# Kernel optimization log

Measured on AMD Instinct MI355X. Metric: run time of the kernel, lower is better.

Reference implementation:

```python
import jax, jax.numpy as jnp
import numpy as np

NB = 5  # frequency bands


def _ln(x, g, b, eps=1e-5):
    m = jnp.mean(x, axis=-1, keepdims=True)
    v = jnp.var(x, axis=-1, keepdims=True)
    return (x - m) / jnp.sqrt(v + eps) * g + b


def _graph_adj(x, adj_w, sw1, sb1, sw2, sb2, pos_factor, pos_enc):
    # x: [B, D, N] -> degree-normalized adjacency [B, N, N]
    d = x.shape[1]
    xt = jnp.swapaxes(x, 1, 2)  # [B, N, D]
    # concat-MLP first layer split: cat(xi, xj) @ W1 == xi @ W1[:d] + xj @ W1[d:]
    a = xt @ sw1[:d]
    bpart = xt @ sw1[d:]
    h = jax.nn.elu(a[:, :, None, :] + bpart[:, None, :, :] + sb1)  # [B, N, N, H]
    dyn = jax.nn.sigmoid(jnp.squeeze(h @ sw2, -1) + sb2)  # [B, N, N]
    static = jax.nn.softmax(adj_w, axis=-1)
    pos = jax.nn.softmax(pos_enc, axis=-1)
    comb = jax.nn.softmax(static + dyn + pos_factor * pos, axis=-1)
    deg = jnp.sum(comb, axis=-1)
    dis = (deg + 1e-8) ** -0.5
    return dis[:, :, None] * comb * dis[:, None, :]


def _gcn(x, adj, w, b):
    # x: [B, D, N], adj: [B, N, N] -> [B, D_out, N]
    xt = jnp.swapaxes(x, 1, 2)
    out = jnp.einsum('bij,bjd->bid', adj, xt) @ w + b
    return jnp.swapaxes(out, 1, 2)


def _mha(x, qkv_w, qkv_b, ow, ob, nh=4):
    B, S, D = x.shape
    dh = D // nh
    q, k, v = jnp.split(x @ qkv_w + qkv_b, 3, axis=-1)
    q = q.reshape(B, S, nh, dh)
    k = k.reshape(B, S, nh, dh)
    v = v.reshape(B, S, nh, dh)
    att = jax.nn.softmax(jnp.einsum('bihd,bjhd->bhij', q, k) / float(np.sqrt(dh)), axis=-1)
    o = jnp.einsum('bhij,bjhd->bihd', att, v).reshape(B, S, D)
    return o @ ow + ob


def setup_inputs():
    key = jax.random.key(0)
    B, D, N = 16, 256, 64
    ks = iter(jax.random.split(key, 40))

    def rn(shape, s=0.05):
        return jax.random.normal(next(ks), shape, dtype=jnp.float32) * s

    eyeN = jnp.eye(N, dtype=jnp.float32)
    return dict(
        feature=jax.random.normal(next(ks), (B, NB * D, 1, N), dtype=jnp.float32),
        l_adj_w=jnp.tile(eyeN[None], (NB, 1, 1)),
        l_sim_w1=rn((NB, 2 * D, D)), l_sim_b1=jnp.zeros((NB, D), jnp.float32),
        l_sim_w2=rn((NB, D, 1)), l_sim_b2=jnp.zeros((NB, 1), jnp.float32),
        l_pos_factor=jnp.full((NB,), 0.5, jnp.float32),
        l_pos_enc=jnp.tile(eyeN[None], (NB, 1, 1)),
        l_gcn_w=rn((NB, D, D)), l_gcn_b=jnp.zeros((NB, D), jnp.float32),
        g_adj_w=jnp.eye(NB, dtype=jnp.float32),
        g_sim_w1=rn((2 * D, D)), g_sim_b1=jnp.zeros((D,), jnp.float32),
        g_sim_w2=rn((D, 1)), g_sim_b2=jnp.zeros((1,), jnp.float32),
        g_pos_factor=jnp.float32(0.5),
        g_pos_enc=jnp.eye(NB, dtype=jnp.float32),
        g_gcn_w=rn((D, D)), g_gcn_b=jnp.zeros((D,), jnp.float32),
        qkv_w=rn((D, 3 * D)), qkv_b=jnp.zeros((3 * D,), jnp.float32),
        attn_ow=rn((D, D)), attn_ob=jnp.zeros((D,), jnp.float32),
        ln1_g=jnp.ones((D,), jnp.float32), ln1_b=jnp.zeros((D,), jnp.float32),
        ln2_g=jnp.ones((D,), jnp.float32), ln2_b=jnp.zeros((D,), jnp.float32),
        mlp_w1=rn((D, 4 * D)), mlp_b1=jnp.zeros((4 * D,), jnp.float32),
        mlp_w2=rn((4 * D, D)), mlp_b2=jnp.zeros((D,), jnp.float32),
        imp_w=rn((NB, N, 1)), imp_b=jnp.zeros((NB, 1), jnp.float32),
    )


def reference(feature, l_adj_w, l_sim_w1, l_sim_b1, l_sim_w2, l_sim_b2,
              l_pos_factor, l_pos_enc, l_gcn_w, l_gcn_b,
              g_adj_w, g_sim_w1, g_sim_b1, g_sim_w2, g_sim_b2,
              g_pos_factor, g_pos_enc, g_gcn_w, g_gcn_b,
              qkv_w, qkv_b, attn_ow, attn_ob,
              ln1_g, ln1_b, ln2_g, ln2_b,
              mlp_w1, mlp_b1, mlp_w2, mlp_b2,
              imp_w, imp_b):
    B = feature.shape[0]
    D = l_gcn_w.shape[-1]
    N = feature.shape[-1]
    # [B, 5*D, 1, N] -> [5, B, D, N] band-major
    x5 = jnp.moveaxis(feature.reshape(B, NB, D, N), 1, 0)
    # per-band local graphs + GCNs (vmapped over the 5 bands)
    local_adj = jax.vmap(_graph_adj)(x5, l_adj_w, l_sim_w1, l_sim_b1,
                                     l_sim_w2, l_sim_b2, l_pos_factor, l_pos_enc)
    local_out = jax.vmap(_gcn)(x5, local_adj, l_gcn_w, l_gcn_b)  # [5, B, D, N]
    scale_nodes = jnp.moveaxis(jnp.mean(local_out, axis=-1), 0, 1)  # [B, 5, D]
    # cross-band attention block (pre: MHA + residual + LN, then MLP + residual + LN)
    attn = _mha(scale_nodes, qkv_w, qkv_b, attn_ow, attn_ob)
    h1 = _ln(scale_nodes + attn, ln1_g, ln1_b)
    mlp = jax.nn.gelu(h1 @ mlp_w1 + mlp_b1, approximate=False) @ mlp_w2 + mlp_b2
    se = _ln(h1 + mlp, ln2_g, ln2_b)  # [B, 5, D]
    # global scale graph over the 5 band nodes
    xg = jnp.swapaxes(se, 1, 2)  # [B, D, 5]
    g_adj = _graph_adj(xg, g_adj_w, g_sim_w1, g_sim_b1, g_sim_w2, g_sim_b2,
                       g_pos_factor, g_pos_enc)
    g_out = jnp.swapaxes(_gcn(xg, g_adj, g_gcn_w, g_gcn_b), 1, 2)  # [B, 5, D]
    # modulate each local band feature by its global scale vector
    enh = local_out * jnp.moveaxis(g_out, 1, 0)[..., None]  # [5, B, D, N]
    # per-band importance projection over channels: [5, B, D, 1]
    out5 = jnp.einsum('kbdn,kno->kbdo', enh, imp_w) + imp_b[:, None, None, :]
    output = jnp.moveaxis(out5, 0, 1).reshape(B, NB * D, 1, 1)
    return output, g_adj, jnp.moveaxis(local_out, 0, 1)
```

## Files before the change

### kernel.cpp

```cpp
#include <hip/hip_runtime.h>
#include <hip/hip_bf16.h>

#define NBANDS 5
#define BATCH  16
#define DIM    256
#define NNODE  64
#define SEQ    5
#define NHEAD  4
#define DHEAD  64

typedef __hip_bfloat16 bf16;
typedef unsigned short ushort_t;
typedef __attribute__((ext_vector_type(8))) short short8;
typedef __attribute__((ext_vector_type(4))) float float4v;

__device__ __forceinline__ float bu2f(ushort_t u){
    bf16 h = *reinterpret_cast<bf16*>(&u);
    return __bfloat162float(h);
}
__device__ __forceinline__ ushort_t f2bu(float x){
    bf16 h = __float2bfloat16(x);
    return *reinterpret_cast<ushort_t*>(&h);
}

__global__ void k_bases(const float* __restrict__ l_adj_w, const float* __restrict__ l_pos_enc,
                        const float* __restrict__ l_pf,
                        const float* __restrict__ g_adj_w, const float* __restrict__ g_pos_enc,
                        const float* __restrict__ g_pf,
                        float* __restrict__ sbase, float* __restrict__ gbase,
                        float* __restrict__ zbuf)
{
    int blk = blockIdx.x;
    int t = threadIdx.x;
    if (blk < NBANDS*NNODE) {
        int k = blk / NNODE, i = blk % NNODE;
        float aw = l_adj_w[(k*NNODE + i)*NNODE + t];
        float pe = l_pos_enc[(k*NNODE + i)*NNODE + t];
        float m1 = aw, m2 = pe;
        for (int o=32;o>0;o>>=1){ m1 = fmaxf(m1, __shfl_xor(m1,o,64)); m2 = fmaxf(m2, __shfl_xor(m2,o,64)); }
        float e1 = __expf(aw-m1), e2 = __expf(pe-m2);
        float s1=e1, s2=e2;
        for (int o=32;o>0;o>>=1){ s1 += __shfl_xor(s1,o,64); s2 += __shfl_xor(s2,o,64); }
        float pf = l_pf[k];
        sbase[(k*NNODE+i)*NNODE + t] = e1/s1 + pf*(e2/s2);
    } else if (blk == NBANDS*NNODE) {
        if (t < NBANDS) {
            int i = t;
            float r1[NBANDS], r2[NBANDS];
            float m1=-1e30f, m2=-1e30f;
            for (int j=0;j<NBANDS;j++){
                r1[j]=g_adj_w[i*NBANDS+j]; r2[j]=g_pos_enc[i*NBANDS+j];
                m1=fmaxf(m1,r1[j]); m2=fmaxf(m2,r2[j]);
            }
            float s1=0.f,s2=0.f;
            for (int j=0;j<NBANDS;j++){ r1[j]=__expf(r1[j]-m1); r2[j]=__expf(r2[j]-m2); s1+=r1[j]; s2+=r2[j]; }
            float pf = g_pf[0];
            for (int j=0;j<NBANDS;j++) gbase[i*NBANDS+j] = r1[j]/s1 + pf*(r2[j]/s2);
        }
    } else {
        for (int i=t;i<DIM;i+=64) zbuf[i] = 0.f;
    }
}

__global__ void k_prep(const float* __restrict__ w1, const float* __restrict__ gw,
                       ushort_t* __restrict__ w1bt, ushort_t* __restrict__ gwbt)
{
    int blk = blockIdx.x;
    int inst = blk >> 4;
    int t = blk & 15;
    int r0 = (t>>2)*64, c0 = (t&3)*64;
    const float* src; ushort_t* dst;
    if (inst < 10){
        int k = inst>>1, half = inst&1;
        src = w1  + ((size_t)k*512 + half*256)*256;
        dst = w1bt+ ((size_t)k*512 + half*256)*256;
    } else {
        int k = inst-10;
        src = gw  + (size_t)k*65536;
        dst = gwbt+ (size_t)k*65536;
    }
    __shared__ ushort_t tile[64][65];
    int tid = threadIdx.x;
    int jj = tid & 63, i4 = tid >> 6;
    for (int p=0;p<16;p++){
        int i = p*4 + i4;
        tile[i][jj] = f2bu(src[(size_t)(r0+i)*256 + c0 + jj]);
    }
    __syncthreads();
    for (int p=0;p<16;p++){
        int i = p*4 + i4;
        dst[(size_t)(c0+i)*256 + r0 + jj] = tile[jj][i];
    }
}

__global__ void k_transpose_feat(const float* __restrict__ feat,
                                 ushort_t* __restrict__ xtb,
                                 ushort_t* __restrict__ xtT)
{
    int k = blockIdx.x / BATCH, b = blockIdx.x % BATCH;
    __shared__ ushort_t tile[64][65];
    const float* src = feat + ((size_t)b*NBANDS*DIM + (size_t)k*DIM)*NNODE;
    ushort_t* dst = xtb + (size_t)(k*BATCH+b)*NNODE*DIM;
    int tid = threadIdx.x;
    ushort_t* dstT = xtT + (size_t)(k*BATCH+b)*DIM*NNODE;
    for (int u=0; u<64; ++u){
        int idx = u*256 + tid;
        dstT[idx] = f2bu(src[idx]);
    }
    for (int dt=0; dt<4; ++dt){
        for (int r=0;r<16;r++){
            int dp = r*4 + (tid>>6);
            int n  = tid & 63;
            tile[dp][n] = f2bu(src[(size_t)(dt*64+dp)*NNODE + n]);
        }
        __syncthreads();
        for (int r=0;r<16;r++){
            int n  = r*4 + (tid>>6);
            int dp = tid & 63;
            dst[(size_t)n*DIM + dt*64 + dp] = tile[dp][n];
        }
        __syncthreads();
    }
}

__global__ void __launch_bounds__(256) k_ab_mfma(const ushort_t* __restrict__ xtb,
                        const ushort_t* __restrict__ w1bt, const float* __restrict__ b1,
                        ushort_t* __restrict__ aab, ushort_t* __restrict__ bbb)
{
    int blk = blockIdx.x;
    int kband = blk / (BATCH*8);
    int b = (blk/8) % BATCH;
    int nblk = blk & 7;
    int tid = threadIdx.x;
    int wave = tid>>6, lane = tid&63;
    int c16 = lane & 15, quad = lane >> 4;
    int m0 = wave*16;
    size_t rowbase = (size_t)(kband*BATCH+b)*NNODE;
    const ushort_t* Aptr = xtb + (rowbase + m0 + c16)*DIM + quad*8;
    const ushort_t* Bbase = w1bt + (size_t)kband*512*DIM;
    int ncol0 = nblk*64;
    const ushort_t* Bptr0 = Bbase + (size_t)(ncol0 +  0 + c16)*DIM + quad*8;
    const ushort_t* Bptr1 = Bbase + (size_t)(ncol0 + 16 + c16)*DIM + quad*8;
    const ushort_t* Bptr2 = Bbase + (size_t)(ncol0 + 32 + c16)*DIM + quad*8;
    const ushort_t* Bptr3 = Bbase + (size_t)(ncol0 + 48 + c16)*DIM + quad*8;
    float4v acc0 = {0.f,0.f,0.f,0.f}, acc1 = acc0, acc2 = acc0, acc3 = acc0;
    #pragma unroll
    for (int ks=0; ks<8; ++ks){
        short8 a  = *reinterpret_cast<const short8*>(Aptr  + ks*32);
        short8 b0 = *reinterpret_cast<const short8*>(Bptr0 + ks*32);
        short8 b1v= *reinterpret_cast<const short8*>(Bptr1 + ks*32);
        short8 b2 = *reinterpret_cast<const short8*>(Bptr2 + ks*32);
        short8 b3 = *reinterpret_cast<const short8*>(Bptr3 + ks*32);
        acc0 = __builtin_amdgcn_mfma_f32_16x16x32_bf16(a, b0, acc0, 0,0,0);
        acc1 = __builtin_amdgcn_mfma_f32_16x16x32_bf16(a, b1v, acc1, 0,0,0);
        acc2 = __builtin_amdgcn_mfma_f32_16x16x32_bf16(a, b2, acc2, 0,0,0);
        acc3 = __builtin_amdgcn_mfma_f32_16x16x32_bf16(a, b3, acc3, 0,0,0);
    }
    int half = nblk >> 2;
    int cbase = (nblk & 3)*64;
    ushort_t* dst = half ? bbb : aab;
    float4v accs[4] = {acc0, acc1, acc2, acc3};
    #pragma unroll
    for (int nt=0; nt<4; ++nt){
        int cg = cbase + nt*16 + c16;
        float bias = half ? 0.f : b1[kband*DIM + cg];
        #pragma unroll
        for (int r=0;r<4;r++){
            int m = m0 + quad*4 + r;
            dst[(rowbase + m)*DIM + cg] = f2bu(accs[nt][r] + bias);
        }
    }
}

__global__ void k_dyn_comb(const ushort_t* __restrict__ aab,
                           const ushort_t* __restrict__ bbb,
                           const float* __restrict__ w2, const float* __restrict__ b2arr,
                           const float* __restrict__ sbase,
                           ushort_t* __restrict__ combb)
{
    int blk = blockIdx.x;
    int k = blk / (BATCH*16);
    int b = (blk / 16) % BATCH;
    int i0 = (blk % 16) * 4;
    int kb = k*BATCH + b;
    __shared__ float arows[4][DIM];
    __shared__ float w2s[DIM];
    __shared__ float dyn_s[4][NNODE];
    int tid = threadIdx.x;
    int wave = tid >> 6, lane = tid & 63;
    for (int r=0;r<4;r++) arows[r][tid] = bu2f(aab[((size_t)kb*NNODE + i0 + r)*DIM + tid]);
    w2s[tid] = w2[k*DIM + tid];
    __syncthreads();
    const ushort_t* bpbase = bbb + (size_t)kb*NNODE*DIM;
    for (int jt=0; jt<16; ++jt){
        int j = jt*4 + wave;
        const ushort_t* bj = bpbase + (size_t)j*DIM;
        float acc[4] = {0.f,0.f,0.f,0.f};
        #pragma unroll
        for (int m=0;m<4;m++){
            int dd = lane + m*64;
            float bpv = bu2f(bj[dd]);
            float wv  = w2s[dd];
            #pragma unroll
            for (int r=0;r<4;r++){
                float v = arows[r][dd] + bpv;
                float e = (v > 0.f) ? v : (__expf(v) - 1.f);
                acc[r] += e*wv;
            }
        }
        #pragma unroll
        for (int r=0;r<4;r++){
            float s = acc[r];
            for (int o=32;o>0;o>>=1) s += __shfl_xor(s,o,64);
            if (lane==0) dyn_s[r][j] = s;
        }
    }
    __syncthreads();
    {
        float sb2 = b2arr[k];
        float t = dyn_s[wave][lane] + sb2;
        float sg = 1.f/(1.f + __expf(-t));
        float val = sbase[(k*NNODE + i0 + wave)*NNODE + lane] + sg;
        float m = val;
        for (int o=32;o>0;o>>=1) m = fmaxf(m, __shfl_xor(m,o,64));
        float e = __expf(val - m);
        float s = e;
        for (int o=32;o>0;o>>=1) s += __shfl_xor(s,o,64);
        combb[((size_t)kb*NNODE + i0 + wave)*NNODE + lane] = f2bu(e/s);
    }
}

__global__ void __launch_bounds__(256) k_y_mfma(const ushort_t* __restrict__ combb,
                       const ushort_t* __restrict__ xtT,
                       ushort_t* __restrict__ yb)
{
    int blk = blockIdx.x;
    int kband = blk / (BATCH*4);
    int b = (blk/4) % BATCH;
    int nblk = blk & 3;
    int tid = threadIdx.x;
    int wave = tid>>6, lane = tid&63;
    int c16 = lane & 15, quad = lane >> 4;
    int m0 = wave*16;
    int kb = kband*BATCH + b;
    const ushort_t* Aptr = combb + ((size_t)kb*NNODE + m0 + c16)*NNODE + quad*8;
    const ushort_t* Bbase = xtT + (size_t)kb*DIM*NNODE;
    int ncol0 = nblk*64;
    const ushort_t* Bptr0 = Bbase + (size_t)(ncol0 +  0 + c16)*NNODE + quad*8;
    const ushort_t* Bptr1 = Bbase + (size_t)(ncol0 + 16 + c16)*NNODE + quad*8;
    const ushort_t* Bptr2 = Bbase + (size_t)(ncol0 + 32 + c16)*NNODE + quad*8;
    const ushort_t* Bptr3 = Bbase + (size_t)(ncol0 + 48 + c16)*NNODE + quad*8;
    float4v acc0 = {0.f,0.f,0.f,0.f}, acc1 = acc0, acc2 = acc0, acc3 = acc0;
    #pragma unroll
    for (int ks=0; ks<2; ++ks){
        short8 a  = *reinterpret_cast<const short8*>(Aptr  + ks*32);
        short8 b0 = *reinterpret_cast<const short8*>(Bptr0 + ks*32);
        short8 b1v= *reinterpret_cast<const short8*>(Bptr1 + ks*32);
        short8 b2 = *reinterpret_cast<const short8*>(Bptr2 + ks*32);
        short8 b3 = *reinterpret_cast<const short8*>(Bptr3 + ks*32);
        acc0 = __builtin_amdgcn_mfma_f32_16x16x32_bf16(a, b0, acc0, 0,0,0);
        acc1 = __builtin_amdgcn_mfma_f32_16x16x32_bf16(a, b1v, acc1, 0,0,0);
        acc2 = __builtin_amdgcn_mfma_f32_16x16x32_bf16(a, b2, acc2, 0,0,0);
        acc3 = __builtin_amdgcn_mfma_f32_16x16x32_bf16(a, b3, acc3, 0,0,0);
    }
    size_t rowbase = (size_t)kb*NNODE;
    float4v accs[4] = {acc0, acc1, acc2, acc3};
    #pragma unroll
    for (int nt=0; nt<4; ++nt){
        int cg = ncol0 + nt*16 + c16;
        #pragma unroll
        for (int r=0;r<4;r++){
            int m = m0 + quad*4 + r;
            yb[(rowbase + m)*DIM + cg] = f2bu(accs[nt][r]);
        }
    }
}

__global__ void __launch_bounds__(256) k_gcn_mfma(const ushort_t* __restrict__ yb,
                         const ushort_t* __restrict__ gwbt, const float* __restrict__ gb,
                         float* __restrict__ out_local)
{
    int blk = blockIdx.x;
    int kband = blk / (BATCH*4);
    int b = (blk/4) % BATCH;
    int nblk = blk & 3;
    int tid = threadIdx.x;
    int wave = tid>>6, lane = tid&63;
    int c16 = lane & 15, quad = lane >> 4;
    int m0 = wave*16;
    int kb = kband*BATCH + b;
    const ushort_t* Aptr = yb + ((size_t)kb*NNODE + m0 + c16)*DIM + quad*8;
    const ushort_t* Bbase = gwbt + (size_t)kband*DIM*DIM;
    int ncol0 = nblk*64;
    const ushort_t* Bptr0 = Bbase + (size_t)(ncol0 +  0 + c16)*DIM + quad*8;
    const ushort_t* Bptr1 = Bbase + (size_t)(ncol0 + 16 + c16)*DIM + quad*8;
    const ushort_t* Bptr2 = Bbase + (size_t)(ncol0 + 32 + c16)*DIM + quad*8;
    const ushort_t* Bptr3 = Bbase + (size_t)(ncol0 + 48 + c16)*DIM + quad*8;
    float4v acc0 = {0.f,0.f,0.f,0.f}, acc1 = acc0, acc2 = acc0, acc3 = acc0;
    #pragma unroll
    for (int ks=0; ks<8; ++ks){
        short8 a  = *reinterpret_cast<const short8*>(Aptr  + ks*32);
        short8 b0 = *reinterpret_cast<const short8*>(Bptr0 + ks*32);
        short8 b1v= *reinterpret_cast<const short8*>(Bptr1 + ks*32);
        short8 b2 = *reinterpret_cast<const short8*>(Bptr2 + ks*32);
        short8 b3 = *reinterpret_cast<const short8*>(Bptr3 + ks*32);
        acc0 = __builtin_amdgcn_mfma_f32_16x16x32_bf16(a, b0, acc0, 0,0,0);
        acc1 = __builtin_amdgcn_mfma_f32_16x16x32_bf16(a, b1v, acc1, 0,0,0);
        acc2 = __builtin_amdgcn_mfma_f32_16x16x32_bf16(a, b2, acc2, 0,0,0);
        acc3 = __builtin_amdgcn_mfma_f32_16x16x32_bf16(a, b3, acc3, 0,0,0);
    }
    float4v accs[4] = {acc0, acc1, acc2, acc3};
    #pragma unroll
    for (int nt=0; nt<4; ++nt){
        int cg = ncol0 + nt*16 + c16;
        float bias = gb[kband*DIM + cg];
        float4 v = make_float4(accs[nt][0]+bias, accs[nt][1]+bias, accs[nt][2]+bias, accs[nt][3]+bias);
        float* dst = out_local + ((size_t)(b*NBANDS + kband)*DIM + cg)*NNODE + m0 + quad*4;
        *reinterpret_cast<float4*>(dst) = v;
    }
}

__global__ void k_scale(const float* __restrict__ out_local, float* __restrict__ scalew)
{
    int k = blockIdx.x / BATCH, b = blockIdx.x % BATCH;
    int d = threadIdx.x;
    const float4* zl = reinterpret_cast<const float4*>(out_local + ((size_t)(b*NBANDS + k)*DIM + d)*NNODE);
    float acc = 0.f;
    #pragma unroll
    for (int q=0;q<16;++q){
        float4 v = zl[q];
        acc += v.x + v.y + v.z + v.w;
    }
    scalew[((size_t)b*SEQ + k)*DIM + d] = acc * (1.f/64.f);
}

template<int COLS, int SLICES>
__global__ void __launch_bounds__(256) k_gemv(const float* __restrict__ x, const float* __restrict__ w,
                       const float* __restrict__ bias, float* __restrict__ out,
                       int K, int N, int act)
{
    int chunks = N / COLS;
    int row = blockIdx.x / chunks;
    int n0 = (blockIdx.x % chunks) * COLS;
    int c = threadIdx.x % COLS, s = threadIdx.x / COLS;
    __shared__ float xs[1024];
    __shared__ float part[SLICES][COLS];
    for (int i = threadIdx.x; i < K; i += 256) xs[i] = x[(size_t)row*K + i];
    __syncthreads();
    int klen = K / SLICES;
    const float* wp = w + (size_t)(s*klen)*N + n0 + c;
    const float* xp = xs + s*klen;
    float acc = 0.f;
    #pragma unroll 8
    for (int i = 0; i < klen; ++i) acc += xp[i] * wp[(size_t)i*N];
    part[s][c] = acc;
    __syncthreads();
    if (s == 0){
        float v = bias[n0+c];
        #pragma unroll
        for (int q=0;q<SLICES;q++) v += part[q][c];
        if (act) v = 0.5f*v*(1.f + erff(v*0.70710678118654752f));
        out[(size_t)row*N + n0 + c] = v;
    }
}

__global__ void k_attn(const float* __restrict__ qkvw, float* __restrict__ ows)
{
    int b = blockIdx.x;
    int tid = threadIdx.x;
    int h = tid >> 6, l = tid & 63;
    __shared__ float att[NHEAD][SEQ][SEQ];
    const float* base = qkvw + (size_t)b*SEQ*3*DIM;
    for (int i=0;i<SEQ;i++){
        float qv = base[(size_t)i*3*DIM + h*DHEAD + l];
        for (int j=0;j<SEQ;j++){
            float kv = base[(size_t)j*3*DIM + DIM + h*DHEAD + l];
            float p = qv * kv;
            for (int o=32;o>0;o>>=1) p += __shfl_xor(p,o,64);
            if (l==0) att[h][i][j] = p * 0.125f;
        }
    }
    __syncthreads();
    if (l == 0){
        for (int i=0;i<SEQ;i++){
            float m=-1e30f;
            for (int j=0;j<SEQ;j++) m = fmaxf(m, att[h][i][j]);
            float e[SEQ]; float s=0.f;
            for (int j=0;j<SEQ;j++){ e[j] = __expf(att[h][i][j]-m); s+=e[j]; }
            for (int j=0;j<SEQ;j++) att[h][i][j] = e[j]/s;
        }
    }
    __syncthreads();
    for (int i=0;i<SEQ;i++){
        float acc=0.f;
        for (int j=0;j<SEQ;j++) acc += att[h][i][j] * base[(size_t)j*3*DIM + 2*DIM + h*DHEAD + l];
        ows[((size_t)b*SEQ + i)*DIM + h*DHEAD + l] = acc;
    }
}

__device__ __forceinline__ float block_ln(float v, int tid, float* red, float g, float bln)
{
    float s = v;
    for (int o=32;o>0;o>>=1) s += __shfl_xor(s,o,64);
    int wave = tid>>6, lane = tid&63;
    if (lane==0) red[wave] = s;
    __syncthreads();
    float mean = (red[0]+red[1]+red[2]+red[3]) * (1.f/DIM);
    float c = v - mean;
    float q = c*c;
    for (int o=32;o>0;o>>=1) q += __shfl_xor(q,o,64);
    __syncthreads();
    if (lane==0) red[wave] = q;
    __syncthreads();
    float var = (red[0]+red[1]+red[2]+red[3]) * (1.f/DIM);
    return c * rsqrtf(var + 1e-5f) * g + bln;
}

__global__ void k_ln(const float* __restrict__ a, const float* __restrict__ r,
                     const float* __restrict__ g, const float* __restrict__ be,
                     float* __restrict__ out)
{
    int row = blockIdx.x;
    int d = threadIdx.x;
    __shared__ float red[4];
    float v = a[(size_t)row*DIM + d] + r[(size_t)row*DIM + d];
    out[(size_t)row*DIM + d] = block_ln(v, d, red, g[d], be[d]);
}

__global__ void k_gadj(const float* __restrict__ gaw, const float* __restrict__ gbw,
                       const float* __restrict__ gw2, const float* __restrict__ gb2,
                       const float* __restrict__ gbase,
                       float* __restrict__ gcombw, float* __restrict__ out_gadj)
{
    int b = blockIdx.x;
    int tid = threadIdx.x;
    int wave = tid>>6, lane = tid&63;
    __shared__ float dyn[SEQ][SEQ];
    __shared__ float w2s[DIM];
    w2s[tid] = gw2[tid];
    __syncthreads();
    for (int p = wave; p < SEQ*SEQ; p += 4){
        int i = p / SEQ, j = p % SEQ;
        const float* gar = gaw + ((size_t)b*SEQ+i)*DIM;
        const float* gbr = gbw + ((size_t)b*SEQ+j)*DIM;
        float acc = 0.f;
        #pragma unroll
        for (int m=0;m<4;m++){
            int dd = lane + m*64;
            float v = gar[dd] + gbr[dd];
            float e = (v>0.f) ? v : (__expf(v)-1.f);
            acc += e * w2s[dd];
        }
        for (int o=32;o>0;o>>=1) acc += __shfl_xor(acc,o,64);
        if (lane==0) dyn[i][j] = acc;
    }
    __syncthreads();
    if (tid < SEQ){
        int i = tid;
        float sb2 = gb2[0];
        float row[SEQ]; float m=-1e30f;
        for (int j=0;j<SEQ;j++){
            float sg = 1.f/(1.f+__expf(-(dyn[i][j]+sb2)));
            row[j] = gbase[i*SEQ+j] + sg;
            m = fmaxf(m,row[j]);
        }
        float ssum=0.f;
        for (int j=0;j<SEQ;j++){ row[j]=__expf(row[j]-m); ssum+=row[j]; }
        for (int j=0;j<SEQ;j++){
            float c = row[j]/ssum;
            gcombw[((size_t)b*SEQ+i)*SEQ + j] = c;
            out_gadj[((size_t)b*SEQ+i)*SEQ + j] = c;
        }
    }
}

__global__ void k_gmix(const float* __restrict__ gcombw, const float* __restrict__ sew,
                       float* __restrict__ trow)
{
    int row = blockIdx.x;
    int b = row / SEQ;
    int d = threadIdx.x;
    float t = 0.f;
    #pragma unroll
    for (int j=0;j<SEQ;j++) t += gcombw[row*SEQ + j] * sew[((size_t)b*SEQ + j)*DIM + d];
    trow[(size_t)row*DIM + d] = t;
}

__global__ void k_final(const float* __restrict__ out_local,
                        const float* __restrict__ goutw,
                        const float* __restrict__ imp_w, const float* __restrict__ imp_b,
                        float* __restrict__ out0)
{
    int b = blockIdx.x / NBANDS, k = blockIdx.x % NBANDS;
    __shared__ float iw[NNODE];
    int d = threadIdx.x;
    if (d < NNODE) iw[d] = imp_w[k*NNODE + d];
    __syncthreads();
    const float4* zl = reinterpret_cast<const float4*>(out_local + ((size_t)(b*NBANDS + k)*DIM + d)*NNODE);
    float acc = 0.f;
    #pragma unroll
    for (int q=0;q<16;++q){
        float4 v = zl[q];
        acc += v.x*iw[q*4] + v.y*iw[q*4+1] + v.z*iw[q*4+2] + v.w*iw[q*4+3];
    }
    float val = goutw[((size_t)b*NBANDS+k)*DIM + d] * acc + imp_b[k];
    out0[((size_t)b*NBANDS+k)*DIM + d] = val;
}

extern "C" void kernel_launch(void* const* d_in, const int* in_sizes, int n_in,
                              void* d_out, int out_size, void* d_ws, size_t ws_size,
                              hipStream_t stream)
{
    const float* feature      = (const float*)d_in[0];
    const float* l_adj_w      = (const float*)d_in[1];
    const float* l_sim_w1     = (const float*)d_in[2];
    const float* l_sim_b1     = (const float*)d_in[3];
    const float* l_sim_w2     = (const float*)d_in[4];
    const float* l_sim_b2     = (const float*)d_in[5];
    const float* l_pos_factor = (const float*)d_in[6];
    const float* l_pos_enc    = (const float*)d_in[7];
    const float* l_gcn_w      = (const float*)d_in[8];
    const float* l_gcn_b      = (const float*)d_in[9];
    const float* g_adj_w      = (const float*)d_in[10];
    const float* g_sim_w1     = (const float*)d_in[11];
    const float* g_sim_b1     = (const float*)d_in[12];
    const float* g_sim_w2     = (const float*)d_in[13];
    const float* g_sim_b2     = (const float*)d_in[14];
    const float* g_pos_factor = (const float*)d_in[15];
    const float* g_pos_enc    = (const float*)d_in[16];
    const float* g_gcn_w      = (const float*)d_in[17];
    const float* g_gcn_b      = (const float*)d_in[18];
    const float* qkv_w        = (const float*)d_in[19];
    const float* qkv_b        = (const float*)d_in[20];
    const float* attn_ow      = (const float*)d_in[21];
    const float* attn_ob      = (const float*)d_in[22];
    const float* ln1_g        = (const float*)d_in[23];
    const float* ln1_b        = (const float*)d_in[24];
    const float* ln2_g        = (const float*)d_in[25];
    const float* ln2_b        = (const float*)d_in[26];
    const float* mlp_w1       = (const float*)d_in[27];
    const float* mlp_b1       = (const float*)d_in[28];
    const float* mlp_w2       = (const float*)d_in[29];
    const float* mlp_b2       = (const float*)d_in[30];
    const float* imp_w        = (const float*)d_in[31];
    const float* imp_b        = (const float*)d_in[32];

    float* out0      = (float*)d_out;
    float* out_gadj  = out0 + (size_t)BATCH*NBANDS*DIM;
    float* out_local = out_gadj + (size_t)BATCH*NBANDS*NBANDS;

    const size_t BIG = (size_t)NBANDS*BATCH*NNODE*DIM;
    ushort_t* xtb   = (ushort_t*)d_ws;
    ushort_t* aab   = xtb + BIG;
    ushort_t* bbb   = aab + BIG;
    ushort_t* xtT   = bbb + BIG;
    ushort_t* yb    = aab;
    ushort_t* w1bt  = xtT + BIG;
    ushort_t* gwbt  = w1bt + (size_t)NBANDS*512*DIM;
    ushort_t* combb = gwbt + (size_t)NBANDS*DIM*DIM;
    float* fp = (float*)(combb + (size_t)NBANDS*BATCH*NNODE*NNODE);
    float* sbase  = fp; fp += NBANDS*NNODE*NNODE;
    float* gbase  = fp; fp += 32;
    float* zbuf   = fp; fp += DIM;
    float* scalew = fp; fp += BATCH*SEQ*DIM;
    float* qkvw   = fp; fp += BATCH*SEQ*3*DIM;
    float* ows    = fp; fp += BATCH*SEQ*DIM;
    float* projw  = fp; fp += BATCH*SEQ*DIM;
    float* h1w    = fp; fp += BATCH*SEQ*DIM;
    float* mhw    = fp; fp += BATCH*SEQ*4*DIM;
    float* m2w    = fp; fp += BATCH*SEQ*DIM;
    float* sew    = fp; fp += BATCH*SEQ*DIM;
    float* gaw    = fp; fp += BATCH*SEQ*DIM;
    float* gbw    = fp; fp += BATCH*SEQ*DIM;
    float* gcombw = fp; fp += 512;
    float* trow   = fp; fp += BATCH*SEQ*DIM;
    float* goutw  = fp; fp += BATCH*SEQ*DIM;

    const int ROWS = BATCH*SEQ;

    k_bases<<<NBANDS*NNODE + 2, 64, 0, stream>>>(l_adj_w, l_pos_enc, l_pos_factor,
                                                 g_adj_w, g_pos_enc, g_pos_factor,
                                                 sbase, gbase, zbuf);
    k_prep<<<240, 256, 0, stream>>>(l_sim_w1, l_gcn_w, w1bt, gwbt);
    k_transpose_feat<<<NBANDS*BATCH, 256, 0, stream>>>(feature, xtb, xtT);
    k_ab_mfma<<<NBANDS*BATCH*8, 256, 0, stream>>>(xtb, w1bt, l_sim_b1, aab, bbb);
    k_dyn_comb<<<NBANDS*BATCH*16, 256, 0, stream>>>(aab, bbb, l_sim_w2, l_sim_b2, sbase, combb);
    k_y_mfma<<<NBANDS*BATCH*4, 256, 0, stream>>>(combb, xtT, yb);
    k_gcn_mfma<<<NBANDS*BATCH*4, 256, 0, stream>>>(yb, gwbt, l_gcn_b, out_local);
    k_scale<<<NBANDS*BATCH, 256, 0, stream>>>(out_local, scalew);
    k_gemv<64,4><<<ROWS*12, 256, 0, stream>>>(scalew, qkv_w, qkv_b, qkvw, 256, 768, 0);
    k_attn<<<BATCH, 256, 0, stream>>>(qkvw, ows);
    k_gemv<64,4><<<ROWS*4, 256, 0, stream>>>(ows, attn_ow, attn_ob, projw, 256, 256, 0);
    k_ln<<<ROWS, 256, 0, stream>>>(projw, scalew, ln1_g, ln1_b, h1w);
    k_gemv<64,4><<<ROWS*16, 256, 0, stream>>>(h1w, mlp_w1, mlp_b1, mhw, 256, 1024, 1);
    k_gemv<32,8><<<ROWS*8, 256, 0, stream>>>(mhw, mlp_w2, mlp_b2, m2w, 1024, 256, 0);
    k_ln<<<ROWS, 256, 0, stream>>>(m2w, h1w, ln2_g, ln2_b, sew);
    k_gemv<64,4><<<ROWS*4, 256, 0, stream>>>(sew, g_sim_w1, g_sim_b1, gaw, 256, 256, 0);
    k_gemv<64,4><<<ROWS*4, 256, 0, stream>>>(sew, g_sim_w1 + (size_t)DIM*DIM, zbuf, gbw, 256, 256, 0);
    k_gadj<<<BATCH, 256, 0, stream>>>(gaw, gbw, g_sim_w2, g_sim_b2, gbase, gcombw, out_gadj);
    k_gmix<<<ROWS, 256, 0, stream>>>(gcombw, sew, trow);
    k_gemv<64,4><<<ROWS*4, 256, 0, stream>>>(trow, g_gcn_w, g_gcn_b, goutw, 256, 256, 0);
    k_final<<<BATCH*NBANDS, 256, 0, stream>>>(out_local, goutw, imp_w, imp_b, out0);
}
```

Measured before the change: 264.7 us.

## Merge prep kernels into one head kernel and fuse the tail into one per-batch kernel

Three setup kernels (bases, weight transposes, feature transpose) become a single launch. That launch also converts all tail weights to bf16. The thirteen tail kernels (scale, gemvs, attention, layernorms, global adjacency, gmix, final) are fused into one kernel with one block per batch, keeping intermediates in shared memory. This removes many launches and global round trips. In exchange the tail runs on only 16 blocks, each streaming about 2MB of bf16 weights serially, and the tail weights are now rounded to bf16.

```diff
diff --git a/kernel.cpp b/kernel.cpp
--- a/kernel.cpp
+++ b/kernel.cpp
@@ -23,17 +23,29 @@
     return *reinterpret_cast<ushort_t*>(&h);
 }
 
-__global__ void k_bases(const float* __restrict__ l_adj_w, const float* __restrict__ l_pos_enc,
-                        const float* __restrict__ l_pf,
-                        const float* __restrict__ g_adj_w, const float* __restrict__ g_pos_enc,
-                        const float* __restrict__ g_pf,
-                        float* __restrict__ sbase, float* __restrict__ gbase,
-                        float* __restrict__ zbuf)
+__global__ void __launch_bounds__(256) k_head(
+    const float* __restrict__ l_adj_w, const float* __restrict__ l_pos_enc,
+    const float* __restrict__ l_pf,
+    const float* __restrict__ g_adj_w, const float* __restrict__ g_pos_enc,
+    const float* __restrict__ g_pf,
+    float* __restrict__ sbase, float* __restrict__ gbase,
+    const float* __restrict__ w1, const float* __restrict__ gw,
+    ushort_t* __restrict__ w1bt, ushort_t* __restrict__ gwbt,
+    const float* __restrict__ feat,
+    ushort_t* __restrict__ xtb, ushort_t* __restrict__ xtT,
+    const float* __restrict__ qkv_w, const float* __restrict__ attn_ow,
+    const float* __restrict__ mlp_w1, const float* __restrict__ mlp_w2,
+    const float* __restrict__ g_sim_w1, const float* __restrict__ g_gcn_w,
+    ushort_t* __restrict__ tailw)
 {
     int blk = blockIdx.x;
-    int t = threadIdx.x;
-    if (blk < NBANDS*NNODE) {
-        int k = blk / NNODE, i = blk % NNODE;
+    int tid = threadIdx.x;
+    __shared__ ushort_t tile[64][65];
+
+    if (blk < 80) {
+        int r = blk*4 + (tid>>6);
+        int k = r >> 6, i = r & 63;
+        int t = tid & 63;
         float aw = l_adj_w[(k*NNODE + i)*NNODE + t];
         float pe = l_pos_enc[(k*NNODE + i)*NNODE + t];
         float m1 = aw, m2 = pe;
@@ -43,9 +55,9 @@
         for (int o=32;o>0;o>>=1){ s1 += __shfl_xor(s1,o,64); s2 += __shfl_xor(s2,o,64); }
         float pf = l_pf[k];
         sbase[(k*NNODE+i)*NNODE + t] = e1/s1 + pf*(e2/s2);
-    } else if (blk == NBANDS*NNODE) {
-        if (t < NBANDS) {
-            int i = t;
+    } else if (blk == 80) {
+        if (tid < NBANDS) {
+            int i = tid;
             float r1[NBANDS], r2[NBANDS];
             float m1=-1e30f, m2=-1e30f;
             for (int j=0;j<NBANDS;j++){
@@ -57,69 +69,68 @@
             float pf = g_pf[0];
             for (int j=0;j<NBANDS;j++) gbase[i*NBANDS+j] = r1[j]/s1 + pf*(r2[j]/s2);
         }
+    } else if (blk < 321) {
+        int idx = blk - 81;
+        int inst = idx >> 4;
+        int t = idx & 15;
+        int r0 = (t>>2)*64, c0 = (t&3)*64;
+        const float* src; ushort_t* dst;
+        if (inst < 10){
+            int k = inst>>1, half = inst&1;
+            src = w1  + ((size_t)k*512 + half*256)*256;
+            dst = w1bt+ ((size_t)k*512 + half*256)*256;
+        } else {
+            int k = inst-10;
+            src = gw  + (size_t)k*65536;
+            dst = gwbt+ (size_t)k*65536;
+        }
+        int jj = tid & 63, i4 = tid >> 6;
+        for (int p=0;p<16;p++){
+            int i = p*4 + i4;
+            tile[i][jj] = f2bu(src[(size_t)(r0+i)*256 + c0 + jj]);
+        }
+        __syncthreads();
+        for (int p=0;p<16;p++){
+            int i = p*4 + i4;
+            dst[(size_t)(c0+i)*256 + r0 + jj] = tile[jj][i];
+        }
+    } else if (blk < 401) {
+        int idx = blk - 321;
+        int k = idx / BATCH, b = idx % BATCH;
+        const float* src = feat + ((size_t)b*NBANDS*DIM + (size_t)k*DIM)*NNODE;
+        ushort_t* dst = xtb + (size_t)(k*BATCH+b)*NNODE*DIM;
+        ushort_t* dstT = xtT + (size_t)(k*BATCH+b)*DIM*NNODE;
+        for (int u=0; u<64; ++u){
+            int i = u*256 + tid;
+            dstT[i] = f2bu(src[i]);
+        }
+        for (int dt=0; dt<4; ++dt){
+            for (int r=0;r<16;r++){
+                int dp = r*4 + (tid>>6);
+                int n  = tid & 63;
+                tile[dp][n] = f2bu(src[(size_t)(dt*64+dp)*NNODE + n]);
+            }
+            __syncthreads();
+            for (int r=0;r<16;r++){
+                int n  = r*4 + (tid>>6);
+                int dp = tid & 63;
+                dst[(size_t)n*DIM + dt*64 + dp] = tile[dp][n];
+            }
+            __syncthreads();
+        }
     } else {
-        for (int i=t;i<DIM;i+=64) zbuf[i] = 0.f;
-    }
-}
-
-__global__ void k_prep(const float* __restrict__ w1, const float* __restrict__ gw,
-                       ushort_t* __restrict__ w1bt, ushort_t* __restrict__ gwbt)
-{
-    int blk = blockIdx.x;
-    int inst = blk >> 4;
-    int t = blk & 15;
-    int r0 = (t>>2)*64, c0 = (t&3)*64;
-    const float* src; ushort_t* dst;
-    if (inst < 10){
-        int k = inst>>1, half = inst&1;
-        src = w1  + ((size_t)k*512 + half*256)*256;
-        dst = w1bt+ ((size_t)k*512 + half*256)*256;
-    } else {
-        int k = inst-10;
-        src = gw  + (size_t)k*65536;
-        dst = gwbt+ (size_t)k*65536;
-    }
-    __shared__ ushort_t tile[64][65];
-    int tid = threadIdx.x;
-    int jj = tid & 63, i4 = tid >> 6;
-    for (int p=0;p<16;p++){
-        int i = p*4 + i4;
-        tile[i][jj] = f2bu(src[(size_t)(r0+i)*256 + c0 + jj]);
-    }
-    __syncthreads();
-    for (int p=0;p<16;p++){
-        int i = p*4 + i4;
-        dst[(size_t)(c0+i)*256 + r0 + jj] = tile[jj][i];
-    }
-}
-
-__global__ void k_transpose_feat(const float* __restrict__ feat,
-                                 ushort_t* __restrict__ xtb,
-                                 ushort_t* __restrict__ xtT)
-{
-    int k = blockIdx.x / BATCH, b = blockIdx.x % BATCH;
-    __shared__ ushort_t tile[64][65];
-    const float* src = feat + ((size_t)b*NBANDS*DIM + (size_t)k*DIM)*NNODE;
-    ushort_t* dst = xtb + (size_t)(k*BATCH+b)*NNODE*DIM;
-    int tid = threadIdx.x;
-    ushort_t* dstT = xtT + (size_t)(k*BATCH+b)*DIM*NNODE;
-    for (int u=0; u<64; ++u){
-        int idx = u*256 + tid;
-        dstT[idx] = f2bu(src[idx]);
-    }
-    for (int dt=0; dt<4; ++dt){
-        for (int r=0;r<16;r++){
-            int dp = r*4 + (tid>>6);
-            int n  = tid & 63;
-            tile[dp][n] = f2bu(src[(size_t)(dt*64+dp)*NNODE + n]);
-        }
-        __syncthreads();
-        for (int r=0;r<16;r++){
-            int n  = r*4 + (tid>>6);
-            int dp = tid & 63;
-            dst[(size_t)n*DIM + dt*64 + dp] = tile[dp][n];
-        }
-        __syncthreads();
+        size_t base = (size_t)(blk-401)*5120;
+        for (int i=0;i<20;i++){
+            size_t gidx = base + (size_t)i*256 + tid;
+            const float* src; size_t off;
+            if (gidx < 196608)      { src=qkv_w;    off=gidx; }
+            else if (gidx < 262144) { src=attn_ow;  off=gidx-196608; }
+            else if (gidx < 524288) { src=mlp_w1;   off=gidx-262144; }
+            else if (gidx < 786432) { src=mlp_w2;   off=gidx-524288; }
+            else if (gidx < 917504) { src=g_sim_w1; off=gidx-786432; }
+            else                    { src=g_gcn_w;  off=gidx-917504; }
+            tailw[gidx] = f2bu(src[off]);
+        }
     }
 }
 
@@ -320,84 +331,6 @@
     }
 }
 
-__global__ void k_scale(const float* __restrict__ out_local, float* __restrict__ scalew)
-{
-    int k = blockIdx.x / BATCH, b = blockIdx.x % BATCH;
-    int d = threadIdx.x;
-    const float4* zl = reinterpret_cast<const float4*>(out_local + ((size_t)(b*NBANDS + k)*DIM + d)*NNODE);
-    float acc = 0.f;
-    #pragma unroll
-    for (int q=0;q<16;++q){
-        float4 v = zl[q];
-        acc += v.x + v.y + v.z + v.w;
-    }
-    scalew[((size_t)b*SEQ + k)*DIM + d] = acc * (1.f/64.f);
-}
-
-template<int COLS, int SLICES>
-__global__ void __launch_bounds__(256) k_gemv(const float* __restrict__ x, const float* __restrict__ w,
-                       const float* __restrict__ bias, float* __restrict__ out,
-                       int K, int N, int act)
-{
-    int chunks = N / COLS;
-    int row = blockIdx.x / chunks;
-    int n0 = (blockIdx.x % chunks) * COLS;
-    int c = threadIdx.x % COLS, s = threadIdx.x / COLS;
-    __shared__ float xs[1024];
-    __shared__ float part[SLICES][COLS];
-    for (int i = threadIdx.x; i < K; i += 256) xs[i] = x[(size_t)row*K + i];
-    __syncthreads();
-    int klen = K / SLICES;
-    const float* wp = w + (size_t)(s*klen)*N + n0 + c;
-    const float* xp = xs + s*klen;
-    float acc = 0.f;
-    #pragma unroll 8
-    for (int i = 0; i < klen; ++i) acc += xp[i] * wp[(size_t)i*N];
-    part[s][c] = acc;
-    __syncthreads();
-    if (s == 0){
-        float v = bias[n0+c];
-        #pragma unroll
-        for (int q=0;q<SLICES;q++) v += part[q][c];
-        if (act) v = 0.5f*v*(1.f + erff(v*0.70710678118654752f));
-        out[(size_t)row*N + n0 + c] = v;
-    }
-}
-
-__global__ void k_attn(const float* __restrict__ qkvw, float* __restrict__ ows)
-{
-    int b = blockIdx.x;
-    int tid = threadIdx.x;
-    int h = tid >> 6, l = tid & 63;
-    __shared__ float att[NHEAD][SEQ][SEQ];
-    const float* base = qkvw + (size_t)b*SEQ*3*DIM;
-    for (int i=0;i<SEQ;i++){
-        float qv = base[(size_t)i*3*DIM + h*DHEAD + l];
-        for (int j=0;j<SEQ;j++){
-            float kv = base[(size_t)j*3*DIM + DIM + h*DHEAD + l];
-            float p = qv * kv;
-            for (int o=32;o>0;o>>=1) p += __shfl_xor(p,o,64);
-            if (l==0) att[h][i][j] = p * 0.125f;
-        }
-    }
-    __syncthreads();
-    if (l == 0){
-        for (int i=0;i<SEQ;i++){
-            float m=-1e30f;
-            for (int j=0;j<SEQ;j++) m = fmaxf(m, att[h][i][j]);
-            float e[SEQ]; float s=0.f;
-            for (int j=0;j<SEQ;j++){ e[j] = __expf(att[h][i][j]-m); s+=e[j]; }
-            for (int j=0;j<SEQ;j++) att[h][i][j] = e[j]/s;
-        }
-    }
-    __syncthreads();
-    for (int i=0;i<SEQ;i++){
-        float acc=0.f;
-        for (int j=0;j<SEQ;j++) acc += att[h][i][j] * base[(size_t)j*3*DIM + 2*DIM + h*DHEAD + l];
-        ows[((size_t)b*SEQ + i)*DIM + h*DHEAD + l] = acc;
-    }
-}
-
 __device__ __forceinline__ float block_ln(float v, int tid, float* red, float g, float bln)
 {
     float s = v;
@@ -416,95 +349,262 @@
     return c * rsqrtf(var + 1e-5f) * g + bln;
 }
 
-__global__ void k_ln(const float* __restrict__ a, const float* __restrict__ r,
-                     const float* __restrict__ g, const float* __restrict__ be,
-                     float* __restrict__ out)
-{
-    int row = blockIdx.x;
-    int d = threadIdx.x;
-    __shared__ float red[4];
-    float v = a[(size_t)row*DIM + d] + r[(size_t)row*DIM + d];
-    out[(size_t)row*DIM + d] = block_ln(v, d, red, g[d], be[d]);
-}
-
-__global__ void k_gadj(const float* __restrict__ gaw, const float* __restrict__ gbw,
-                       const float* __restrict__ gw2, const float* __restrict__ gb2,
-                       const float* __restrict__ gbase,
-                       float* __restrict__ gcombw, float* __restrict__ out_gadj)
-{
+__global__ void __launch_bounds__(256) k_tail(
+    const float* __restrict__ out_local,
+    const ushort_t* __restrict__ tailw,
+    const float* __restrict__ qkv_bias, const float* __restrict__ ob,
+    const float* __restrict__ ln1_g, const float* __restrict__ ln1_b,
+    const float* __restrict__ mb1, const float* __restrict__ mb2,
+    const float* __restrict__ ln2_g, const float* __restrict__ ln2_b,
+    const float* __restrict__ gb1,
+    const float* __restrict__ gw2, const float* __restrict__ gb2,
+    const float* __restrict__ gbase,
+    const float* __restrict__ ggb,
+    const float* __restrict__ imp_w, const float* __restrict__ imp_b,
+    float* __restrict__ out0, float* __restrict__ out_gadj)
+{
+    const ushort_t* qkvb = tailw;
+    const ushort_t* owb  = qkvb + 196608;
+    const ushort_t* w1b  = owb  + 65536;
+    const ushort_t* w2b  = w1b  + 262144;
+    const ushort_t* gw1b = w2b  + 262144;
+    const ushort_t* ggwb = gw1b + 131072;
+
     int b = blockIdx.x;
     int tid = threadIdx.x;
     int wave = tid>>6, lane = tid&63;
+
+    __shared__ float pool[11840];
+    float* iw    = pool;
+    float* impd  = pool + 320;
+    float* sc    = pool + 1600;
+    float* qkv   = pool + 2880;
+    float* oatt  = pool + 6720;
+    float* h1    = pool + 8000;
+    float* mh    = pool + 2880;
+    float* sew   = pool + 1600;
+    float* ga    = pool + 9280;
+    float* gb_   = pool + 10560;
+    float* goutL = pool + 2880;
+    float* tt5   = pool + 4160;
+    __shared__ float att[NHEAD][SEQ][SEQ];
     __shared__ float dyn[SEQ][SEQ];
-    __shared__ float w2s[DIM];
-    w2s[tid] = gw2[tid];
-    __syncthreads();
-    for (int p = wave; p < SEQ*SEQ; p += 4){
-        int i = p / SEQ, j = p % SEQ;
-        const float* gar = gaw + ((size_t)b*SEQ+i)*DIM;
-        const float* gbr = gbw + ((size_t)b*SEQ+j)*DIM;
+    __shared__ float gcomb[SEQ][SEQ];
+    __shared__ float red[4];
+
+    if (tid < 64){
+        #pragma unroll
+        for (int k=0;k<5;k++) iw[k*64+tid] = imp_w[k*64+tid];
+    }
+    __syncthreads();
+
+    for (int k=0;k<5;k++){
+        const float4* zl = reinterpret_cast<const float4*>(
+            out_local + ((size_t)(b*NBANDS+k)*DIM + tid)*NNODE);
+        const float* iwk = iw + k*64;
+        float s=0.f, di=0.f;
+        #pragma unroll
+        for (int q=0;q<16;q++){
+            float4 v = zl[q];
+            s  += v.x + v.y + v.z + v.w;
+            di += v.x*iwk[q*4] + v.y*iwk[q*4+1] + v.z*iwk[q*4+2] + v.w*iwk[q*4+3];
+        }
+        sc[k*DIM+tid]   = s * (1.f/64.f);
+        impd[k*DIM+tid] = di;
+    }
+    __syncthreads();
+
+    {
+        float a0[5]={0,0,0,0,0}, a1[5]={0,0,0,0,0}, a2[5]={0,0,0,0,0};
+        for (int kk=0; kk<DIM; ++kk){
+            float w0 = bu2f(qkvb[(size_t)kk*768 + tid]);
+            float w1v= bu2f(qkvb[(size_t)kk*768 + 256 + tid]);
+            float w2v= bu2f(qkvb[(size_t)kk*768 + 512 + tid]);
+            #pragma unroll
+            for (int s=0;s<5;s++){
+                float xv = sc[s*DIM + kk];
+                a0[s] += xv*w0; a1[s] += xv*w1v; a2[s] += xv*w2v;
+            }
+        }
+        float b0 = qkv_bias[tid], b1v = qkv_bias[256+tid], b2v = qkv_bias[512+tid];
+        #pragma unroll
+        for (int s=0;s<5;s++){
+            qkv[s*768 + tid]       = a0[s] + b0;
+            qkv[s*768 + 256 + tid] = a1[s] + b1v;
+            qkv[s*768 + 512 + tid] = a2[s] + b2v;
+        }
+    }
+    __syncthreads();
+
+    {
+        int h = wave, l = lane;
+        for (int i=0;i<5;i++){
+            float qv = qkv[i*768 + h*64 + l];
+            for (int j=0;j<5;j++){
+                float kv = qkv[j*768 + 256 + h*64 + l];
+                float p = qv*kv;
+                for (int o=32;o>0;o>>=1) p += __shfl_xor(p,o,64);
+                if (l==0) att[h][i][j] = p*0.125f;
+            }
+        }
+        __syncthreads();
+        if (l==0){
+            for (int i=0;i<5;i++){
+                float m=-1e30f;
+                for (int j=0;j<5;j++) m = fmaxf(m, att[h][i][j]);
+                float e[5]; float ssum=0.f;
+                for (int j=0;j<5;j++){ e[j]=__expf(att[h][i][j]-m); ssum+=e[j]; }
+                for (int j=0;j<5;j++) att[h][i][j]=e[j]/ssum;
+            }
+        }
+        __syncthreads();
+        for (int i=0;i<5;i++){
+            float acc=0.f;
+            for (int j=0;j<5;j++) acc += att[h][i][j]*qkv[j*768 + 512 + h*64 + l];
+            oatt[i*DIM + h*64 + l] = acc;
+        }
+    }
+    __syncthreads();
+
+    {
+        float pa[5]={0,0,0,0,0};
+        for (int dp=0; dp<DIM; ++dp){
+            float w = bu2f(owb[(size_t)dp*DIM + tid]);
+            #pragma unroll
+            for (int s=0;s<5;s++) pa[s] += oatt[s*DIM+dp]*w;
+        }
+        float obv = ob[tid], g = ln1_g[tid], be = ln1_b[tid];
+        for (int s=0;s<5;s++){
+            float v = pa[s] + obv + sc[s*DIM+tid];
+            float o = block_ln(v, tid, red, g, be);
+            h1[s*DIM+tid] = o;
+            __syncthreads();
+        }
+    }
+
+    {
+        float ma[20];
+        #pragma unroll
+        for (int i=0;i<20;i++) ma[i]=0.f;
+        for (int dp=0; dp<DIM; ++dp){
+            float w0 = bu2f(w1b[(size_t)dp*1024 + tid]);
+            float w1v= bu2f(w1b[(size_t)dp*1024 + 256 + tid]);
+            float w2v= bu2f(w1b[(size_t)dp*1024 + 512 + tid]);
+            float w3 = bu2f(w1b[(size_t)dp*1024 + 768 + tid]);
+            #pragma unroll
+            for (int s=0;s<5;s++){
+                float xv = h1[s*DIM+dp];
+                ma[s*4+0] += xv*w0; ma[s*4+1] += xv*w1v;
+                ma[s*4+2] += xv*w2v; ma[s*4+3] += xv*w3;
+            }
+        }
+        float bb[4] = {mb1[tid], mb1[256+tid], mb1[512+tid], mb1[768+tid]};
+        #pragma unroll
+        for (int s=0;s<5;s++){
+            #pragma unroll
+            for (int c=0;c<4;c++){
+                float v = ma[s*4+c] + bb[c];
+                mh[s*1024 + c*256 + tid] = 0.5f*v*(1.f + erff(v*0.70710678118654752f));
+            }
+        }
+    }
+    __syncthreads();
+
+    {
+        float sa[5]={0,0,0,0,0};
+        for (int dp=0; dp<1024; ++dp){
+            float w = bu2f(w2b[(size_t)dp*DIM + tid]);
+            #pragma unroll
+            for (int s=0;s<5;s++) sa[s] += mh[s*1024+dp]*w;
+        }
+        float bv = mb2[tid], g = ln2_g[tid], be = ln2_b[tid];
+        for (int s=0;s<5;s++){
+            float v = sa[s] + bv + h1[s*DIM+tid];
+            float o = block_ln(v, tid, red, g, be);
+            __syncthreads();
+            sew[s*DIM+tid] = o;
+            __syncthreads();
+        }
+    }
+
+    {
+        float aA[5]={0,0,0,0,0}, aB[5]={0,0,0,0,0};
+        for (int dp=0; dp<DIM; ++dp){
+            float wA = bu2f(gw1b[(size_t)dp*DIM + tid]);
+            float wB = bu2f(gw1b[(size_t)(DIM+dp)*DIM + tid]);
+            #pragma unroll
+            for (int s=0;s<5;s++){
+                float xv = sew[s*DIM+dp];
+                aA[s] += xv*wA; aB[s] += xv*wB;
+            }
+        }
+        float b1v = gb1[tid];
+        #pragma unroll
+        for (int s=0;s<5;s++){
+            ga[s*DIM+tid]  = aA[s] + b1v;
+            gb_[s*DIM+tid] = aB[s];
+        }
+    }
+    __syncthreads();
+
+    for (int p=wave; p<25; p+=4){
+        int i = p/5, j = p%5;
         float acc = 0.f;
         #pragma unroll
         for (int m=0;m<4;m++){
             int dd = lane + m*64;
-            float v = gar[dd] + gbr[dd];
+            float v = ga[i*DIM+dd] + gb_[j*DIM+dd];
             float e = (v>0.f) ? v : (__expf(v)-1.f);
-            acc += e * w2s[dd];
+            acc += e * gw2[dd];
         }
         for (int o=32;o>0;o>>=1) acc += __shfl_xor(acc,o,64);
         if (lane==0) dyn[i][j] = acc;
     }
     __syncthreads();
-    if (tid < SEQ){
+    if (tid < 5){
         int i = tid;
         float sb2 = gb2[0];
-        float row[SEQ]; float m=-1e30f;
-        for (int j=0;j<SEQ;j++){
+        float row[5]; float m=-1e30f;
+        for (int j=0;j<5;j++){
             float sg = 1.f/(1.f+__expf(-(dyn[i][j]+sb2)));
-            row[j] = gbase[i*SEQ+j] + sg;
+            row[j] = gbase[i*5+j] + sg;
             m = fmaxf(m,row[j]);
         }
         float ssum=0.f;
-        for (int j=0;j<SEQ;j++){ row[j]=__expf(row[j]-m); ssum+=row[j]; }
-        for (int j=0;j<SEQ;j++){
+        for (int j=0;j<5;j++){ row[j]=__expf(row[j]-m); ssum+=row[j]; }
+        for (int j=0;j<5;j++){
             float c = row[j]/ssum;
-            gcombw[((size_t)b*SEQ+i)*SEQ + j] = c;
-            out_gadj[((size_t)b*SEQ+i)*SEQ + j] = c;
-        }
-    }
-}
-
-__global__ void k_gmix(const float* __restrict__ gcombw, const float* __restrict__ sew,
-                       float* __restrict__ trow)
-{
-    int row = blockIdx.x;
-    int b = row / SEQ;
-    int d = threadIdx.x;
-    float t = 0.f;
+            gcomb[i][j] = c;
+            out_gadj[((size_t)b*5+i)*5 + j] = c;
+        }
+    }
+    __syncthreads();
+
+    {
+        #pragma unroll
+        for (int k=0;k<5;k++){
+            float t = 0.f;
+            #pragma unroll
+            for (int j=0;j<5;j++) t += gcomb[k][j]*sew[j*DIM+tid];
+            tt5[k*DIM+tid] = t;
+        }
+        __syncthreads();
+        float ga5[5]={0,0,0,0,0};
+        for (int dp=0; dp<DIM; ++dp){
+            float w = bu2f(ggwb[(size_t)dp*DIM + tid]);
+            #pragma unroll
+            for (int k=0;k<5;k++) ga5[k] += tt5[k*DIM+dp]*w;
+        }
+        float bv = ggb[tid];
+        #pragma unroll
+        for (int k=0;k<5;k++) goutL[k*DIM+tid] = ga5[k] + bv;
+    }
+    __syncthreads();
+
     #pragma unroll
-    for (int j=0;j<SEQ;j++) t += gcombw[row*SEQ + j] * sew[((size_t)b*SEQ + j)*DIM + d];
-    trow[(size_t)row*DIM + d] = t;
-}
-
-__global__ void k_final(const float* __restrict__ out_local,
-                        const float* __restrict__ goutw,
-                        const float* __restrict__ imp_w, const float* __restrict__ imp_b,
-                        float* __restrict__ out0)
-{
-    int b = blockIdx.x / NBANDS, k = blockIdx.x % NBANDS;
-    __shared__ float iw[NNODE];
-    int d = threadIdx.x;
-    if (d < NNODE) iw[d] = imp_w[k*NNODE + d];
-    __syncthreads();
-    const float4* zl = reinterpret_cast<const float4*>(out_local + ((size_t)(b*NBANDS + k)*DIM + d)*NNODE);
-    float acc = 0.f;
-    #pragma unroll
-    for (int q=0;q<16;++q){
-        float4 v = zl[q];
-        acc += v.x*iw[q*4] + v.y*iw[q*4+1] + v.z*iw[q*4+2] + v.w*iw[q*4+3];
-    }
-    float val = goutw[((size_t)b*NBANDS+k)*DIM + d] * acc + imp_b[k];
-    out0[((size_t)b*NBANDS+k)*DIM + d] = val;
+    for (int k=0;k<5;k++){
+        out0[((size_t)(b*5+k))*DIM + tid] = goutL[k*DIM+tid]*impd[k*DIM+tid] + imp_b[k];
+    }
 }
 
 extern "C" void kernel_launch(void* const* d_in, const int* in_sizes, int n_in,
@@ -558,47 +658,26 @@
     ushort_t* w1bt  = xtT + BIG;
     ushort_t* gwbt  = w1bt + (size_t)NBANDS*512*DIM;
     ushort_t* combb = gwbt + (size_t)NBANDS*DIM*DIM;
-    float* fp = (float*)(combb + (size_t)NBANDS*BATCH*NNODE*NNODE);
+    ushort_t* tailw = combb + (size_t)NBANDS*BATCH*NNODE*NNODE;
+    float* fp = (float*)(tailw + 983040);
     float* sbase  = fp; fp += NBANDS*NNODE*NNODE;
     float* gbase  = fp; fp += 32;
-    float* zbuf   = fp; fp += DIM;
-    float* scalew = fp; fp += BATCH*SEQ*DIM;
-    float* qkvw   = fp; fp += BATCH*SEQ*3*DIM;
-    float* ows    = fp; fp += BATCH*SEQ*DIM;
-    float* projw  = fp; fp += BATCH*SEQ*DIM;
-    float* h1w    = fp; fp += BATCH*SEQ*DIM;
-    float* mhw    = fp; fp += BATCH*SEQ*4*DIM;
-    float* m2w    = fp; fp += BATCH*SEQ*DIM;
-    float* sew    = fp; fp += BATCH*SEQ*DIM;
-    float* gaw    = fp; fp += BATCH*SEQ*DIM;
-    float* gbw    = fp; fp += BATCH*SEQ*DIM;
-    float* gcombw = fp; fp += 512;
-    float* trow   = fp; fp += BATCH*SEQ*DIM;
-    float* goutw  = fp; fp += BATCH*SEQ*DIM;
-
-    const int ROWS = BATCH*SEQ;
-
-    k_bases<<<NBANDS*NNODE + 2, 64, 0, stream>>>(l_adj_w, l_pos_enc, l_pos_factor,
-                                                 g_adj_w, g_pos_enc, g_pos_factor,
-                                                 sbase, gbase, zbuf);
-    k_prep<<<240, 256, 0, stream>>>(l_sim_w1, l_gcn_w, w1bt, gwbt);
-    k_transpose_feat<<<NBANDS*BATCH, 256, 0, stream>>>(feature, xtb, xtT);
+
+    k_head<<<593, 256, 0, stream>>>(l_adj_w, l_pos_enc, l_pos_factor,
+                                    g_adj_w, g_pos_enc, g_pos_factor,
+                                    sbase, gbase,
+                                    l_sim_w1, l_gcn_w, w1bt, gwbt,
+                                    feature, xtb, xtT,
+                                    qkv_w, attn_ow, mlp_w1, mlp_w2, g_sim_w1, g_gcn_w,
+                                    tailw);
     k_ab_mfma<<<NBANDS*BATCH*8, 256, 0, stream>>>(xtb, w1bt, l_sim_b1, aab, bbb);
     k_dyn_comb<<<NBANDS*BATCH*16, 256, 0, stream>>>(aab, bbb, l_sim_w2, l_sim_b2, sbase, combb);
     k_y_mfma<<<NBANDS*BATCH*4, 256, 0, stream>>>(combb, xtT, yb);
     k_gcn_mfma<<<NBANDS*BATCH*4, 256, 0, stream>>>(yb, gwbt, l_gcn_b, out_local);
-    k_scale<<<NBANDS*BATCH, 256, 0, stream>>>(out_local, scalew);
-    k_gemv<64,4><<<ROWS*12, 256, 0, stream>>>(scalew, qkv_w, qkv_b, qkvw, 256, 768, 0);
-    k_attn<<<BATCH, 256, 0, stream>>>(qkvw, ows);
-    k_gemv<64,4><<<ROWS*4, 256, 0, stream>>>(ows, attn_ow, attn_ob, projw, 256, 256, 0);
-    k_ln<<<ROWS, 256, 0, stream>>>(projw, scalew, ln1_g, ln1_b, h1w);
-    k_gemv<64,4><<<ROWS*16, 256, 0, stream>>>(h1w, mlp_w1, mlp_b1, mhw, 256, 1024, 1);
-    k_gemv<32,8><<<ROWS*8, 256, 0, stream>>>(mhw, mlp_w2, mlp_b2, m2w, 1024, 256, 0);
-    k_ln<<<ROWS, 256, 0, stream>>>(m2w, h1w, ln2_g, ln2_b, sew);
-    k_gemv<64,4><<<ROWS*4, 256, 0, stream>>>(sew, g_sim_w1, g_sim_b1, gaw, 256, 256, 0);
-    k_gemv<64,4><<<ROWS*4, 256, 0, stream>>>(sew, g_sim_w1 + (size_t)DIM*DIM, zbuf, gbw, 256, 256, 0);
-    k_gadj<<<BATCH, 256, 0, stream>>>(gaw, gbw, g_sim_w2, g_sim_b2, gbase, gcombw, out_gadj);
-    k_gmix<<<ROWS, 256, 0, stream>>>(gcombw, sew, trow);
-    k_gemv<64,4><<<ROWS*4, 256, 0, stream>>>(trow, g_gcn_w, g_gcn_b, goutw, 256, 256, 0);
-    k_final<<<BATCH*NBANDS, 256, 0, stream>>>(out_local, goutw, imp_w, imp_b, out0);
-}
+    k_tail<<<BATCH, 256, 0, stream>>>(out_local, tailw,
+                                      qkv_b, attn_ob, ln1_g, ln1_b,
+                                      mlp_b1, mlp_b2, ln2_g, ln2_b,
+                                      g_sim_b1, g_sim_w2, g_sim_b2, gbase,
+                                      g_gcn_b, imp_w, imp_b,
+                                      out0, out_gadj);
+}
```

Measured after the change: 360.5 us. 1.36x slower.
